# Performance work log

Hardware: AMD Instinct MI355X
Metric: run time of the kernel (lower is better)

Reference implementation:

```python
import jax, jax.numpy as jnp
import numpy as np

B, L, D, NH = 4, 1500, 512, 8
HD = D // NH
EPS = 1e-8            # F.normalize eps
PEPS = 1.1920929e-07  # torch clamp_probs eps for float32
TEMP = 1.0


def setup_inputs():
    key = jax.random.key(0)
    ks = jax.random.split(key, 12)
    s = 1.0 / np.sqrt(D)
    eye = jnp.eye(D, dtype=jnp.float32)
    return {
        "hidden": jax.random.normal(ks[0], (B, L, D), jnp.float32),
        "lengths": jnp.ones((B,), jnp.float32),
        "u_noise": jax.random.uniform(ks[1], (B, L), jnp.float32),
        "W1": jax.random.normal(ks[2], (D, D), jnp.float32) * s,
        "b1": jnp.zeros((D,), jnp.float32),
        "W2": jax.random.normal(ks[3], (D, D), jnp.float32) * s,
        "b2": jnp.zeros((D,), jnp.float32),
        "Wq": eye + jax.random.normal(ks[4], (D, D), jnp.float32) * 0.01,
        "Wk": eye + jax.random.normal(ks[5], (D, D), jnp.float32) * 0.01,
        "sim_bias": jnp.float32(0.098),
        "learned_query": jax.random.normal(ks[6], (D,), jnp.float32),
        "Wpk": eye + jax.random.normal(ks[7], (D, D), jnp.float32) * 0.01,
        "Wpv": eye + jax.random.normal(ks[8], (D, D), jnp.float32) * 0.01,
        "Wpo": eye + jax.random.normal(ks[9], (D, D), jnp.float32) * 0.01,
        "ln_g": jnp.ones((D,), jnp.float32),
        "ln_b": jnp.zeros((D,), jnp.float32),
    }


def reference(hidden, lengths, u_noise, W1, b1, W2, b2, Wq, Wk, sim_bias,
              learned_query, Wpk, Wpv, Wpo, ln_g, ln_b):
    Bb, Ll, Dd = hidden.shape

    def nrm(x):
        n = jnp.sqrt(jnp.sum(x * x, -1, keepdims=True))
        return x / jnp.maximum(n, EPS)

    def mlp(x):
        return jax.nn.gelu(x @ W1.T + b1, approximate=False) @ W2.T + b2

    # boundary logits from adjacent-frame cosine similarity (dropout = eval identity)
    q_in = nrm(hidden[:, :-1]); q = nrm(mlp(q_in) + q_in) @ Wq.T
    k_in = nrm(hidden[:, 1:]);  k = nrm(mlp(k_in) + k_in) @ Wk.T
    cos = jnp.sum(q * k, -1)                                   # (B, L-1)
    probs = jnp.clip((1.0 - (cos + sim_bias)) * 0.5, 0.0, 1.0)
    probs = jnp.pad(probs, ((0, 0), (0, 1)))                   # (B, L)

    # RelaxedBernoulli rsample with explicit logistic noise
    p = jnp.clip(probs, PEPS, 1.0 - PEPS)
    u = jnp.clip(u_noise, PEPS, 1.0 - PEPS)
    soft = jax.nn.sigmoid((jnp.log(p) - jnp.log1p(-p) + jnp.log(u) - jnp.log1p(-u)) / TEMP)
    hard = (soft > 0.5).astype(hidden.dtype)

    idx = jnp.arange(Ll)
    valid_len = jnp.minimum((lengths * (Ll + 1)).astype(jnp.int32) - 1, Ll)
    trunc = (valid_len < Ll)[:, None]
    zmask = trunc & (idx[None] >= valid_len[:, None])
    omask = trunc & (idx[None] == valid_len[:, None])
    soft = jnp.where(omask, 1.0, jnp.where(zmask, 0.0, soft))
    hard = jnp.where(omask, 1.0, jnp.where(zmask, 0.0, hard))
    hard_b = hard - jax.lax.stop_gradient(soft) + soft         # straight-through
    # emergency boundary for all-zero rows
    no_b = (jnp.sum(hard, 1) == 0)[:, None]
    hard_b = jnp.where(no_b & (idx[None] == jnp.minimum(valid_len, Ll - 1)[:, None]), 1.0, hard_b)

    # segment membership (common()): token l in segment s iff exclusive cumsum == s
    seg = jnp.cumsum(hard_b, 1) - hard_b                       # (B, L)
    lmask = idx[None] < (lengths * Ll).astype(jnp.int32)[:, None]
    seg_mask = (seg[:, :, None] == idx[None, None, :].astype(hidden.dtype)) & lmask[:, :, None]  # (B,L,S)

    # layernorm + K/V projections
    mu = jnp.mean(hidden, -1, keepdims=True)
    hv = hidden - mu
    hn = hv / jnp.sqrt(jnp.mean(hv * hv, -1, keepdims=True) + 1e-5) * ln_g + ln_b
    keys = (hn @ Wpk.T).reshape(Bb, Ll, NH, HD)
    vals = (hn @ Wpv.T).reshape(Bb, Ll, NH, HD)

    # query is shared across segments -> scores only differ via the segment mask
    qh = learned_query.reshape(NH, HD)
    base = jnp.einsum('hd,blhd->bhl', qh, keys) * (HD ** -0.5)  # (B,H,L)
    mask_t = jnp.transpose(seg_mask, (0, 2, 1))[:, None]        # (B,1,S,L)
    sc = jnp.where(mask_t, base[:, :, None, :], -jnp.inf)       # (B,H,S,L)
    aw = jnp.nan_to_num(jax.nn.softmax(sc, axis=-1))            # empty segments -> 0 rows
    pooled = jnp.einsum('bhsl,blhd->bshd', aw, vals).reshape(Bb, Ll, Dd)
    return pooled @ Wpo.T                                       # (B, S=L, D)
```

## Files before the change

kernel.cpp:

```cpp
#include <hip/hip_runtime.h>
#include <math.h>

#define Bz 4
#define Lz 1500
#define Dz 512
#define NHz 8
#define Nz (Bz*Lz)
#define PEPSf 1.1920929e-07f

typedef __bf16 bf16x8 __attribute__((ext_vector_type(8)));
typedef unsigned short u16x8 __attribute__((ext_vector_type(8)));
typedef float f32x4 __attribute__((ext_vector_type(4)));
typedef unsigned short us;

__device__ __forceinline__ us f2bf(float f) {
  unsigned u = __float_as_uint(f);
  return (us)((u + 0x7fffu + ((u >> 16) & 1u)) >> 16);
}
__device__ __forceinline__ float bf2f(us b) {
  return __uint_as_float(((unsigned)b) << 16);
}
__device__ __forceinline__ int ti_idx(int row, int col) {
  return (((row >> 4) * 64 + (col >> 3)) << 7) + ((row & 15) << 3) + (col & 7);
}
__device__ __forceinline__ void st_tiled(us* __restrict__ P, int row, int col, us v) {
  P[ti_idx(row, col)] = v;
}

__device__ __forceinline__ bool decode_blk(int bx, int ncg, int& R, int& cg) {
  int xcd = bx & 7, v = bx >> 3;
  cg = v % ncg;
  R = (v / ncg) * 8 + xcd;
  return R < 94;
}

__global__ __launch_bounds__(256) void k_wconv(
    const float* __restrict__ s0, const float* __restrict__ s1, const float* __restrict__ s2,
    const float* __restrict__ s3,
    const float* __restrict__ Wq, const float* __restrict__ Wk,
    const float* __restrict__ Wpk, const float* __restrict__ lq,
    us* __restrict__ h0, us* __restrict__ h1, us* __restrict__ h2, us* __restrict__ h3,
    us* __restrict__ l0, us* __restrict__ l1,
    us* __restrict__ WkTh, us* __restrict__ WkTl, us* __restrict__ WqTh, us* __restrict__ WqTl,
    float* __restrict__ wqe) {
  const int rt = blockIdx.x, mat = blockIdx.y, t = threadIdx.x;
  if (mat == 8) {
    if (rt < 8) {
      for (int d = t; d < Dz; d += 256) {
        float acc = 0.f;
        for (int e = 0; e < 64; ++e) acc += lq[rt * 64 + e] * Wpk[(size_t)(rt * 64 + e) * Dz + d];
        wqe[rt * Dz + d] = acc;
      }
    }
    return;
  }
  const float* S; us* H; us* L = nullptr; bool tr = false;
  switch (mat) {
    case 0: S = s0; H = h0; L = l0; break;
    case 1: S = s1; H = h1; L = l1; break;
    case 2: S = s2; H = h2; break;
    case 3: S = s3; H = h3; break;
    case 4: S = Wk; H = WkTh; L = WkTl; tr = true; break;
    default: S = Wq; H = WqTh; L = WqTl; tr = true; break;
  }
  for (int e = t; e < 8192; e += 256) {
    int mm = e >> 9, c = e & 511;
    float x = tr ? S[(size_t)c * 512 + (rt * 16 + mm)]
                 : S[(size_t)(rt * 16 + mm) * 512 + c];
    us hb = f2bf(x);
    int off = ((rt * 64 + (c >> 3)) << 7) + (mm << 3) + (c & 7);
    H[off] = hb;
    if (L) L[off] = f2bf(x - bf2f(hb));
  }
}

__global__ __launch_bounds__(256) void k_rowprep(const float* __restrict__ h,
    const float* __restrict__ g, const float* __restrict__ bb,
    const float* __restrict__ wqe,
    us* __restrict__ Uh, us* __restrict__ Ul, us* __restrict__ HNh,
    float* __restrict__ base) {
  const int row = blockIdx.x;
  const int t = threadIdx.x;
  const float* x = h + (size_t)row * Dz;
  float x0 = x[t], x1 = x[t + 256];
  float s = x0 + x1, q = x0 * x0 + x1 * x1;
  #pragma unroll
  for (int o = 32; o > 0; o >>= 1) { s += __shfl_xor(s, o, 64); q += __shfl_xor(q, o, 64); }
  __shared__ float ls[4], lq[4];
  __shared__ float xs[Dz];
  if ((t & 63) == 0) { ls[t >> 6] = s; lq[t >> 6] = q; }
  __syncthreads();
  s = ls[0] + ls[1] + ls[2] + ls[3];
  q = lq[0] + lq[1] + lq[2] + lq[3];
  float un = 1.f / fmaxf(sqrtf(q), 1e-8f);
  float u0 = x0 * un, u1 = x1 * un;
  us hb0 = f2bf(u0), hb1 = f2bf(u1);
  st_tiled(Uh, row, t, hb0);       st_tiled(Ul, row, t, f2bf(u0 - bf2f(hb0)));
  st_tiled(Uh, row, t + 256, hb1); st_tiled(Ul, row, t + 256, f2bf(u1 - bf2f(hb1)));
  float mu = s * (1.f / 512.f);
  float var = fmaxf(q * (1.f / 512.f) - mu * mu, 0.f);
  float r = rsqrtf(var + 1e-5f);
  float hn0 = (x0 - mu) * r * g[t] + bb[t];
  float hn1 = (x1 - mu) * r * g[t + 256] + bb[t + 256];
  st_tiled(HNh, row, t, f2bf(hn0));
  st_tiled(HNh, row, t + 256, f2bf(hn1));
  xs[t] = hn0; xs[t + 256] = hn1;
  __syncthreads();
  const int hh = t >> 5, lane = t & 31;
  float accb = 0.f;
  for (int d = lane; d < Dz; d += 32) accb += xs[d] * wqe[hh * Dz + d];
  #pragma unroll
  for (int o = 16; o > 0; o >>= 1) accb += __shfl_xor(accb, o, 32);
  if (lane == 0) base[(size_t)row * NHz + hh] = accb * 0.125f;
}

template<int SPLIT>
__device__ __forceinline__ void gemm_body(
    const us* __restrict__ Ah, const us* __restrict__ Al,
    const us* __restrict__ Bh, const us* __restrict__ Bl,
    const float* __restrict__ bias,
    const us* __restrict__ addH, const us* __restrict__ addL, int doGelu,
    float* __restrict__ outF, us* __restrict__ outH, us* __restrict__ outL,
    int R, int cg, int colbase, int Nrows) {
  const int t = threadIdx.x, w = t >> 6, l = t & 63;
  const int m = l & 15, q = l >> 4;
  const int wr = w & 1, wc = w >> 1;
  const int laneoff = q * 128 + m * 8;
  const int nrtm1 = (Nrows >> 4) - 1;

  const u16x8* pa[2]; const u16x8* pal[2];
  const u16x8* pb[2]; const u16x8* pbl[2];
  #pragma unroll
  for (int i = 0; i < 2; ++i) {
    int rt = min(R * 4 + wr * 2 + i, nrtm1);
    pa[i] = (const u16x8*)(Ah + (size_t)rt * 8192 + laneoff);
    if (SPLIT == 3) pal[i] = (const u16x8*)(Al + (size_t)rt * 8192 + laneoff);
  }
  #pragma unroll
  for (int j = 0; j < 2; ++j) {
    int ct = cg * 4 + wc * 2 + j;
    pb[j] = (const u16x8*)(Bh + (size_t)ct * 8192 + laneoff);
    if (SPLIT == 3) pbl[j] = (const u16x8*)(Bl + (size_t)ct * 8192 + laneoff);
  }

  u16x8 bAh[2][2], bAl[2][2], bBh[2][2], bBl[2][2];
  #pragma unroll
  for (int i = 0; i < 2; ++i) {
    bAh[0][i] = pa[i][0];
    if (SPLIT == 3) bAl[0][i] = pal[i][0];
  }
  #pragma unroll
  for (int j = 0; j < 2; ++j) {
    bBh[0][j] = pb[j][0];
    if (SPLIT == 3) bBl[0][j] = pbl[j][0];
  }

  f32x4 acc[2][2];
  #pragma unroll
  for (int i = 0; i < 2; ++i)
    #pragma unroll
    for (int j = 0; j < 2; ++j) acc[i][j] = (f32x4){0.f, 0.f, 0.f, 0.f};

  #pragma unroll 2
  for (int s = 0; s < 16; ++s) {
    const int cur = s & 1, nxt = cur ^ 1;
    const int sn = (s + 1) & 15;
    #pragma unroll
    for (int i = 0; i < 2; ++i) {
      bAh[nxt][i] = pa[i][sn * 64];
      if (SPLIT == 3) bAl[nxt][i] = pal[i][sn * 64];
    }
    #pragma unroll
    for (int j = 0; j < 2; ++j) {
      bBh[nxt][j] = pb[j][sn * 64];
      if (SPLIT == 3) bBl[nxt][j] = pbl[j][sn * 64];
    }
    #pragma unroll
    for (int i = 0; i < 2; ++i)
      #pragma unroll
      for (int j = 0; j < 2; ++j) {
        bf16x8 a = __builtin_bit_cast(bf16x8, bAh[cur][i]);
        bf16x8 b = __builtin_bit_cast(bf16x8, bBh[cur][j]);
        acc[i][j] = __builtin_amdgcn_mfma_f32_16x16x32_bf16(a, b, acc[i][j], 0, 0, 0);
        if (SPLIT == 3) {
          bf16x8 al_ = __builtin_bit_cast(bf16x8, bAl[cur][i]);
          bf16x8 bl_ = __builtin_bit_cast(bf16x8, bBl[cur][j]);
          acc[i][j] = __builtin_amdgcn_mfma_f32_16x16x32_bf16(a, bl_, acc[i][j], 0, 0, 0);
          acc[i][j] = __builtin_amdgcn_mfma_f32_16x16x32_bf16(al_, b, acc[i][j], 0, 0, 0);
        }
      }
  }

  const int row0 = R * 64 + wr * 32;
  const int col0 = colbase + wc * 32;
  #pragma unroll
  for (int i = 0; i < 2; ++i) {
    #pragma unroll
    for (int r = 0; r < 4; ++r) {
      const int grow = row0 + i * 16 + q * 4 + r;
      if (grow >= Nrows) continue;
      #pragma unroll
      for (int j = 0; j < 2; ++j) {
        const int gcol = col0 + j * 16 + m;
        float v = acc[i][j][r];
        if (bias)   v += bias[gcol];
        if (addH) {
          int ai = ti_idx(grow, gcol);
          v += bf2f(addH[ai]) + bf2f(addL[ai]);
        }
        if (doGelu) v = 0.5f * v * (1.f + erff(v * 0.70710678118654752f));
        if (outF) outF[(size_t)grow * Dz + gcol] = v;
        if (outH) {
          us hb = f2bf(v);
          st_tiled(outH, grow, gcol, hb);
          if (outL) st_tiled(outL, grow, gcol, f2bf(v - bf2f(hb)));
        }
      }
    }
  }
}

__global__ __launch_bounds__(256, 4) void g_t1_vals_gt(
    const us* Uh, const us* Ul, const us* W1h, const us* W1l, const float* b1, us* T1h, us* T1l,
    const us* HNh, const us* Wpvh, float* VALS,
    const us* WkTh, const us* WkTl, const us* WqTh, const us* WqTl, us* Gth, us* Gtl) {
  if (blockIdx.z == 2) {
    int bx = blockIdx.x;
    if (bx >= 64) return;
    gemm_body<3>(WkTh, WkTl, WqTh, WqTl, nullptr, nullptr, nullptr, 0,
                 nullptr, Gth, Gtl, bx >> 3, bx & 7, (bx & 7) * 64, 512);
    return;
  }
  int R, cg;
  if (!decode_blk(blockIdx.x, 8, R, cg)) return;
  if (blockIdx.z == 0)
    gemm_body<3>(Uh, Ul, W1h, W1l, b1, nullptr, nullptr, 1,
                 nullptr, T1h, T1l, R, cg, cg * 64, Nz);
  else
    gemm_body<1>(HNh, nullptr, Wpvh, nullptr, nullptr, nullptr, nullptr, 0,
                 VALS, nullptr, nullptr, R, cg, cg * 64, Nz);
}

__global__ __launch_bounds__(256, 4) void g_w2(
    const us* T1h, const us* T1l, const us* W2h, const us* W2l, const float* b2,
    const us* Uh, const us* Ul, float* M, us* Mh, us* Ml) {
  int R, cg;
  if (!decode_blk(blockIdx.x, 8, R, cg)) return;
  gemm_body<3>(T1h, T1l, W2h, W2l, b2, Uh, Ul, 0, M, Mh, Ml, R, cg, cg * 64, Nz);
}

__global__ __launch_bounds__(256, 4) void g_p(
    const us* Mh, const us* Ml, const us* Gth, const us* Gtl, float* P) {
  int R, cg;
  if (!decode_blk(blockIdx.x, 8, R, cg)) return;
  gemm_body<3>(Mh, Ml, Gth, Gtl, nullptr, nullptr, nullptr, 0,
               P, nullptr, nullptr, R, cg, cg * 64, Nz);
}

__global__ __launch_bounds__(256, 4) void g_out(
    const us* Ph, const us* Wpoh, float* out) {
  int R, cg;
  if (!decode_blk(blockIdx.x, 8, R, cg)) return;
  gemm_body<1>(Ph, nullptr, Wpoh, nullptr, nullptr, nullptr, nullptr, 0,
               out, nullptr, nullptr, R, cg, cg * 64, Nz);
}

__global__ __launch_bounds__(256) void k_probs(const float* __restrict__ P,
    const float* __restrict__ M, const float* __restrict__ simb,
    float* __restrict__ probs) {
  const int w = threadIdx.x >> 6, t = threadIdx.x & 63;
  const int l = blockIdx.x * 4 + w, b = blockIdx.y;
  if (l >= Lz) return;
  if (l == Lz - 1) { if (t == 0) probs[(size_t)b * Lz + l] = 0.f; return; }
  const float* pp = P + ((size_t)b * Lz + l) * Dz;
  const float* m0 = M + ((size_t)b * Lz + l) * Dz;
  const float* m1 = M + ((size_t)b * Lz + l + 1) * Dz;
  float accd = 0.f, q0 = 0.f, q1 = 0.f;
  for (int i = t; i < Dz; i += 64) {
    float a = pp[i], x0 = m0[i], x1 = m1[i];
    accd += a * x1; q0 += x0 * x0; q1 += x1 * x1;
  }
  #pragma unroll
  for (int o = 32; o > 0; o >>= 1) {
    accd += __shfl_xor(accd, o, 64);
    q0 += __shfl_xor(q0, o, 64);
    q1 += __shfl_xor(q1, o, 64);
  }
  if (t == 0) {
    float un0 = 1.f / fmaxf(sqrtf(q0), 1e-8f);
    float un1 = 1.f / fmaxf(sqrtf(q1), 1e-8f);
    float cosv = accd * un0 * un1;
    float p = (1.f - (cosv + simb[0])) * 0.5f;
    probs[(size_t)b * Lz + l] = fminf(fmaxf(p, 0.f), 1.f);
  }
}

__global__ __launch_bounds__(256) void k_boundary(const float* __restrict__ probs,
    const float* __restrict__ un, const float* __restrict__ lengths,
    int* __restrict__ seg_start, int* __restrict__ seg_meta) {
  const int b = blockIdx.x, t = threadIdx.x;
  __shared__ float hard[Lz];
  __shared__ float ps[256];
  __shared__ float ws4[4];
  const float len = lengths[b];
  const int valid_len = min((int)(len * (Lz + 1)) - 1, Lz);
  const int Lm = (int)(len * Lz);
  const bool trunc = valid_len < Lz;
  for (int l = t; l < Lz; l += 256) {
    float p = probs[(size_t)b * Lz + l];
    p = fminf(fmaxf(p, PEPSf), 1.f - PEPSf);
    float u = un[(size_t)b * Lz + l];
    u = fminf(fmaxf(u, PEPSf), 1.f - PEPSf);
    float z = logf(p) - log1pf(-p) + logf(u) - log1pf(-u);
    float soft = 1.f / (1.f + expf(-z));
    float hd = soft > 0.5f ? 1.f : 0.f;
    if (trunc && l >= valid_len) hd = (l == valid_len) ? 1.f : 0.f;
    hard[l] = hd;
  }
  __syncthreads();
  float sm = 0.f;
  for (int l = t; l < Lz; l += 256) sm += hard[l];
  #pragma unroll
  for (int o = 32; o > 0; o >>= 1) sm += __shfl_xor(sm, o, 64);
  if ((t & 63) == 0) ws4[t >> 6] = sm;
  __syncthreads();
  float total = ws4[0] + ws4[1] + ws4[2] + ws4[3];
  if (total == 0.f && t == 0) hard[min(valid_len, Lz - 1)] = 1.f;
  __syncthreads();
  const int l0 = t * 6;
  float loc = 0.f;
  for (int i = 0; i < 6; ++i) { int l = l0 + i; if (l < Lz) loc += hard[l]; }
  ps[t] = loc;
  __syncthreads();
  for (int off = 1; off < 256; off <<= 1) {
    float v = (t >= off) ? ps[t - off] : 0.f;
    __syncthreads();
    ps[t] += v;
    __syncthreads();
  }
  float run = ps[t] - loc;
  for (int i = 0; i < 6; ++i) {
    int l = l0 + i; if (l >= Lz) break;
    int seg = (int)(run + 0.5f);
    if (l == 0) seg_start[b * (Lz + 1) + 0] = 0;
    else if (hard[l - 1] > 0.5f) seg_start[b * (Lz + 1) + seg] = l;
    if (l == Lz - 1) {
      int nseg = seg + 1;
      seg_meta[b * 2 + 0] = nseg;
      seg_meta[b * 2 + 1] = Lm;
      seg_start[b * (Lz + 1) + nseg] = Lz;
    }
    run += hard[l];
  }
}

__global__ __launch_bounds__(256) void k_pool(const float* __restrict__ base,
    const float* __restrict__ VALS, const int* __restrict__ seg_start,
    const int* __restrict__ seg_meta, us* __restrict__ Ph) {
  const int s = blockIdx.x, b = blockIdx.y, t = threadIdx.x;
  const int orow = b * Lz + s;
  const int nseg = seg_meta[b * 2], Lm = seg_meta[b * 2 + 1];
  int start = 0, end = 0;
  bool empty = true;
  if (s < nseg) {
    start = seg_start[b * (Lz + 1) + s];
    end = min(seg_start[b * (Lz + 1) + s + 1], Lm);
    empty = start >= end;
  }
  if (empty) { st_tiled(Ph, orow, t, 0); st_tiled(Ph, orow, t + 256, 0); return; }
  const int h = t >> 5, lane = t & 31;
  const float* bp = base + (size_t)b * Lz * NHz + h;
  float m = -1e30f;
  for (int l = start + lane; l < end; l += 32) m = fmaxf(m, bp[(size_t)l * NHz]);
  #pragma unroll
  for (int o = 16; o > 0; o >>= 1) m = fmaxf(m, __shfl_xor(m, o, 32));
  float den = 0.f;
  for (int l = start + lane; l < end; l += 32) den += expf(bp[(size_t)l * NHz] - m);
  #pragma unroll
  for (int o = 16; o > 0; o >>= 1) den += __shfl_xor(den, o, 32);
  float a0 = 0.f, a1 = 0.f;
  const float* vp = VALS + (size_t)b * Lz * Dz + h * 64 + lane;
  for (int l = start; l < end; ++l) {
    float wgt = expf(bp[(size_t)l * NHz] - m);
    a0 += wgt * vp[(size_t)l * Dz];
    a1 += wgt * vp[(size_t)l * Dz + 32];
  }
  float inv = 1.f / den;
  st_tiled(Ph, orow, h * 64 + lane, f2bf(a0 * inv));
  st_tiled(Ph, orow, h * 64 + lane + 32, f2bf(a1 * inv));
}

extern "C" void kernel_launch(void* const* d_in, const int* in_sizes, int n_in,
                              void* d_out, int out_size, void* d_ws, size_t ws_size,
                              hipStream_t stream) {
  const float* hidden  = (const float*)d_in[0];
  const float* lengths = (const float*)d_in[1];
  const float* unoise  = (const float*)d_in[2];
  const float* W1  = (const float*)d_in[3];
  const float* b1  = (const float*)d_in[4];
  const float* W2  = (const float*)d_in[5];
  const float* b2  = (const float*)d_in[6];
  const float* Wq  = (const float*)d_in[7];
  const float* Wk  = (const float*)d_in[8];
  const float* simb   = (const float*)d_in[9];
  const float* lquery = (const float*)d_in[10];
  const float* Wpk = (const float*)d_in[11];
  const float* Wpv = (const float*)d_in[12];
  const float* Wpo = (const float*)d_in[13];
  const float* lng = (const float*)d_in[14];
  const float* lnb = (const float*)d_in[15];
  float* out = (float*)d_out;

  char* p = (char*)d_ws;
  const size_t SF = (size_t)Nz * Dz * 4;
  const size_t TP = (size_t)376 * 8192 * 2;
  const size_t WP = (size_t)32 * 8192 * 2;
  float* M    = (float*)p; p += SF;
  float* PF   = (float*)p; p += SF;
  float* VALS = (float*)p; p += SF;
  us* Uh  = (us*)p; p += TP;
  us* Ul  = (us*)p; p += TP;
  us* T1h = (us*)p; p += TP;
  us* T1l = (us*)p; p += TP;
  us* Mh  = (us*)p; p += TP;
  us* Ml  = (us*)p; p += TP;
  us* HNh = (us*)p; p += TP;
  us* Ph  = (us*)p; p += TP;
  us* W1h = (us*)p; p += WP;
  us* W1l = (us*)p; p += WP;
  us* W2h = (us*)p; p += WP;
  us* W2l = (us*)p; p += WP;
  us* Wpvh = (us*)p; p += WP;
  us* Wpoh = (us*)p; p += WP;
  us* WkTh = (us*)p; p += WP;
  us* WkTl = (us*)p; p += WP;
  us* WqTh = (us*)p; p += WP;
  us* WqTl = (us*)p; p += WP;
  us* Gth  = (us*)p; p += WP;
  us* Gtl  = (us*)p; p += WP;
  float* probs  = (float*)p; p += 24064;
  float* base   = (float*)p; p += 192000;
  int* segst    = (int*)p;   p += 24064;
  int* segmeta  = (int*)p;   p += 256;
  float* wqe    = (float*)p;

  const int G8 = 8 * 12 * 8;

  k_wconv<<<dim3(32, 9), 256, 0, stream>>>(W1, W2, Wpv, Wpo, Wq, Wk, Wpk, lquery,
      W1h, W2h, Wpvh, Wpoh, W1l, W2l, WkTh, WkTl, WqTh, WqTl, wqe);
  k_rowprep<<<Nz, 256, 0, stream>>>(hidden, lng, lnb, wqe, Uh, Ul, HNh, base);
  g_t1_vals_gt<<<dim3(G8, 1, 3), 256, 0, stream>>>(Uh, Ul, W1h, W1l, b1, T1h, T1l,
      HNh, Wpvh, VALS, WkTh, WkTl, WqTh, WqTl, Gth, Gtl);
  g_w2<<<G8, 256, 0, stream>>>(T1h, T1l, W2h, W2l, b2, Uh, Ul, M, Mh, Ml);
  g_p<<<G8, 256, 0, stream>>>(Mh, Ml, Gth, Gtl, PF);
  k_probs<<<dim3(375, Bz), 256, 0, stream>>>(PF, M, simb, probs);
  k_boundary<<<Bz, 256, 0, stream>>>(probs, unoise, lengths, segst, segmeta);
  k_pool<<<dim3(Lz, Bz), 256, 0, stream>>>(base, VALS, segst, segmeta, Ph);
  g_out<<<G8, 256, 0, stream>>>(Ph, Wpoh, out);
}
```

Before: 233.9 us.

## Merge weight conversion with row prep and compute attention scores inside pooling

The weight-conversion and row-prep kernels become one launch, with the first blocks handling weights and the rest handling rows. Because row prep no longer depends on wqe, the per-row base scores are no longer computed there. Instead k_pool recomputes each token's score from the bf16 layernormed rows (HNh) and wqe, twice per token (once for the max pass, once for the weighted sum). The denominator is also folded into the value-accumulation loop. This removes one launch and the base buffer, but it adds redundant dot products, uses bf16 instead of fp32 inputs for the scores, and uses serial per-token loops in pooling.

After: 245.4 us. +4.9%, slower.

```diff
diff --git a/kernel.cpp b/kernel.cpp
--- a/kernel.cpp
+++ b/kernel.cpp
@@ -34,64 +34,62 @@
   return R < 94;
 }
 
-__global__ __launch_bounds__(256) void k_wconv(
-    const float* __restrict__ s0, const float* __restrict__ s1, const float* __restrict__ s2,
-    const float* __restrict__ s3,
+__global__ __launch_bounds__(256) void k_prep(
+    const float* __restrict__ W1, const float* __restrict__ W2,
+    const float* __restrict__ Wpv, const float* __restrict__ Wpo,
     const float* __restrict__ Wq, const float* __restrict__ Wk,
     const float* __restrict__ Wpk, const float* __restrict__ lq,
-    us* __restrict__ h0, us* __restrict__ h1, us* __restrict__ h2, us* __restrict__ h3,
-    us* __restrict__ l0, us* __restrict__ l1,
+    const float* __restrict__ hidden, const float* __restrict__ g, const float* __restrict__ bb,
+    us* __restrict__ W1h, us* __restrict__ W2h, us* __restrict__ Wpvh, us* __restrict__ Wpoh,
+    us* __restrict__ W1l, us* __restrict__ W2l,
     us* __restrict__ WkTh, us* __restrict__ WkTl, us* __restrict__ WqTh, us* __restrict__ WqTl,
-    float* __restrict__ wqe) {
-  const int rt = blockIdx.x, mat = blockIdx.y, t = threadIdx.x;
-  if (mat == 8) {
-    if (rt < 8) {
-      for (int d = t; d < Dz; d += 256) {
-        float acc = 0.f;
-        for (int e = 0; e < 64; ++e) acc += lq[rt * 64 + e] * Wpk[(size_t)(rt * 64 + e) * Dz + d];
-        wqe[rt * Dz + d] = acc;
+    float* __restrict__ wqe,
+    us* __restrict__ Uh, us* __restrict__ Ul, us* __restrict__ HNh) {
+  const int t = threadIdx.x;
+  const int bx = blockIdx.x;
+  if (bx < 224) {
+    const int rt = bx & 31, mat = bx >> 5;
+    if (mat == 6) {
+      if (rt < 8) {
+        for (int d = t; d < Dz; d += 256) {
+          float acc = 0.f;
+          for (int e = 0; e < 64; ++e) acc += lq[rt * 64 + e] * Wpk[(size_t)(rt * 64 + e) * Dz + d];
+          wqe[rt * Dz + d] = acc;
+        }
       }
+      return;
+    }
+    const float* S; us* H; us* L = nullptr; bool tr = false;
+    switch (mat) {
+      case 0: S = W1;  H = W1h;  L = W1l; break;
+      case 1: S = W2;  H = W2h;  L = W2l; break;
+      case 2: S = Wpv; H = Wpvh; break;
+      case 3: S = Wpo; H = Wpoh; break;
+      case 4: S = Wk;  H = WkTh; L = WkTl; tr = true; break;
+      default: S = Wq; H = WqTh; L = WqTl; tr = true; break;
+    }
+    for (int e = t; e < 8192; e += 256) {
+      int mm = e >> 9, c = e & 511;
+      float x = tr ? S[(size_t)c * 512 + (rt * 16 + mm)]
+                   : S[(size_t)(rt * 16 + mm) * 512 + c];
+      us hb = f2bf(x);
+      int off = ((rt * 64 + (c >> 3)) << 7) + (mm << 3) + (c & 7);
+      H[off] = hb;
+      if (L) L[off] = f2bf(x - bf2f(hb));
     }
     return;
   }
-  const float* S; us* H; us* L = nullptr; bool tr = false;
-  switch (mat) {
-    case 0: S = s0; H = h0; L = l0; break;
-    case 1: S = s1; H = h1; L = l1; break;
-    case 2: S = s2; H = h2; break;
-    case 3: S = s3; H = h3; break;
-    case 4: S = Wk; H = WkTh; L = WkTl; tr = true; break;
-    default: S = Wq; H = WqTh; L = WqTl; tr = true; break;
-  }
-  for (int e = t; e < 8192; e += 256) {
-    int mm = e >> 9, c = e & 511;
-    float x = tr ? S[(size_t)c * 512 + (rt * 16 + mm)]
-                 : S[(size_t)(rt * 16 + mm) * 512 + c];
-    us hb = f2bf(x);
-    int off = ((rt * 64 + (c >> 3)) << 7) + (mm << 3) + (c & 7);
-    H[off] = hb;
-    if (L) L[off] = f2bf(x - bf2f(hb));
-  }
-}
-
-__global__ __launch_bounds__(256) void k_rowprep(const float* __restrict__ h,
-    const float* __restrict__ g, const float* __restrict__ bb,
-    const float* __restrict__ wqe,
-    us* __restrict__ Uh, us* __restrict__ Ul, us* __restrict__ HNh,
-    float* __restrict__ base) {
-  const int row = blockIdx.x;
-  const int t = threadIdx.x;
-  const float* x = h + (size_t)row * Dz;
+  const int row = bx - 224;
+  const float* x = hidden + (size_t)row * Dz;
   float x0 = x[t], x1 = x[t + 256];
   float s = x0 + x1, q = x0 * x0 + x1 * x1;
   #pragma unroll
   for (int o = 32; o > 0; o >>= 1) { s += __shfl_xor(s, o, 64); q += __shfl_xor(q, o, 64); }
-  __shared__ float ls[4], lq[4];
-  __shared__ float xs[Dz];
-  if ((t & 63) == 0) { ls[t >> 6] = s; lq[t >> 6] = q; }
+  __shared__ float ls[4], lqs[4];
+  if ((t & 63) == 0) { ls[t >> 6] = s; lqs[t >> 6] = q; }
   __syncthreads();
   s = ls[0] + ls[1] + ls[2] + ls[3];
-  q = lq[0] + lq[1] + lq[2] + lq[3];
+  q = lqs[0] + lqs[1] + lqs[2] + lqs[3];
   float un = 1.f / fmaxf(sqrtf(q), 1e-8f);
   float u0 = x0 * un, u1 = x1 * un;
   us hb0 = f2bf(u0), hb1 = f2bf(u1);
@@ -104,14 +102,6 @@
   float hn1 = (x1 - mu) * r * g[t + 256] + bb[t + 256];
   st_tiled(HNh, row, t, f2bf(hn0));
   st_tiled(HNh, row, t + 256, f2bf(hn1));
-  xs[t] = hn0; xs[t + 256] = hn1;
-  __syncthreads();
-  const int hh = t >> 5, lane = t & 31;
-  float accb = 0.f;
-  for (int d = lane; d < Dz; d += 32) accb += xs[d] * wqe[hh * Dz + d];
-  #pragma unroll
-  for (int o = 16; o > 0; o >>= 1) accb += __shfl_xor(accb, o, 32);
-  if (lane == 0) base[(size_t)row * NHz + hh] = accb * 0.125f;
 }
 
 template<int SPLIT>
@@ -354,7 +344,8 @@
   }
 }
 
-__global__ __launch_bounds__(256) void k_pool(const float* __restrict__ base,
+__global__ __launch_bounds__(256) void k_pool(const us* __restrict__ HNh,
+    const float* __restrict__ wqe,
     const float* __restrict__ VALS, const int* __restrict__ seg_start,
     const int* __restrict__ seg_meta, us* __restrict__ Ph) {
   const int s = blockIdx.x, b = blockIdx.y, t = threadIdx.x;
@@ -369,19 +360,30 @@
   }
   if (empty) { st_tiled(Ph, orow, t, 0); st_tiled(Ph, orow, t + 256, 0); return; }
   const int h = t >> 5, lane = t & 31;
-  const float* bp = base + (size_t)b * Lz * NHz + h;
+  float wq[16];
+  #pragma unroll
+  for (int o = 0; o < 16; ++o) wq[o] = wqe[h * Dz + o * 32 + lane];
   float m = -1e30f;
-  for (int l = start + lane; l < end; l += 32) m = fmaxf(m, bp[(size_t)l * NHz]);
-  #pragma unroll
-  for (int o = 16; o > 0; o >>= 1) m = fmaxf(m, __shfl_xor(m, o, 32));
-  float den = 0.f;
-  for (int l = start + lane; l < end; l += 32) den += expf(bp[(size_t)l * NHz] - m);
-  #pragma unroll
-  for (int o = 16; o > 0; o >>= 1) den += __shfl_xor(den, o, 32);
-  float a0 = 0.f, a1 = 0.f;
+  for (int l = start; l < end; ++l) {
+    const int grow = b * Lz + l;
+    float acc = 0.f;
+    #pragma unroll
+    for (int o = 0; o < 16; ++o) acc += bf2f(HNh[ti_idx(grow, o * 32 + lane)]) * wq[o];
+    #pragma unroll
+    for (int o2 = 16; o2 > 0; o2 >>= 1) acc += __shfl_xor(acc, o2, 32);
+    m = fmaxf(m, acc * 0.125f);
+  }
+  float den = 0.f, a0 = 0.f, a1 = 0.f;
   const float* vp = VALS + (size_t)b * Lz * Dz + h * 64 + lane;
   for (int l = start; l < end; ++l) {
-    float wgt = expf(bp[(size_t)l * NHz] - m);
+    const int grow = b * Lz + l;
+    float acc = 0.f;
+    #pragma unroll
+    for (int o = 0; o < 16; ++o) acc += bf2f(HNh[ti_idx(grow, o * 32 + lane)]) * wq[o];
+    #pragma unroll
+    for (int o2 = 16; o2 > 0; o2 >>= 1) acc += __shfl_xor(acc, o2, 32);
+    float wgt = expf(acc * 0.125f - m);
+    den += wgt;
     a0 += wgt * vp[(size_t)l * Dz];
     a1 += wgt * vp[(size_t)l * Dz + 32];
   }
@@ -439,22 +441,21 @@
   us* Gth  = (us*)p; p += WP;
   us* Gtl  = (us*)p; p += WP;
   float* probs  = (float*)p; p += 24064;
-  float* base   = (float*)p; p += 192000;
   int* segst    = (int*)p;   p += 24064;
   int* segmeta  = (int*)p;   p += 256;
   float* wqe    = (float*)p;
 
   const int G8 = 8 * 12 * 8;
 
-  k_wconv<<<dim3(32, 9), 256, 0, stream>>>(W1, W2, Wpv, Wpo, Wq, Wk, Wpk, lquery,
-      W1h, W2h, Wpvh, Wpoh, W1l, W2l, WkTh, WkTl, WqTh, WqTl, wqe);
-  k_rowprep<<<Nz, 256, 0, stream>>>(hidden, lng, lnb, wqe, Uh, Ul, HNh, base);
+  k_prep<<<224 + Nz, 256, 0, stream>>>(W1, W2, Wpv, Wpo, Wq, Wk, Wpk, lquery,
+      hidden, lng, lnb,
+      W1h, W2h, Wpvh, Wpoh, W1l, W2l, WkTh, WkTl, WqTh, WqTl, wqe, Uh, Ul, HNh);
   g_t1_vals_gt<<<dim3(G8, 1, 3), 256, 0, stream>>>(Uh, Ul, W1h, W1l, b1, T1h, T1l,
       HNh, Wpvh, VALS, WkTh, WkTl, WqTh, WqTl, Gth, Gtl);
   g_w2<<<G8, 256, 0, stream>>>(T1h, T1l, W2h, W2l, b2, Uh, Ul, M, Mh, Ml);
   g_p<<<G8, 256, 0, stream>>>(Mh, Ml, Gth, Gtl, PF);
   k_probs<<<dim3(375, Bz), 256, 0, stream>>>(PF, M, simb, probs);
   k_boundary<<<Bz, 256, 0, stream>>>(probs, unoise, lengths, segst, segmeta);
-  k_pool<<<dim3(Lz, Bz), 256, 0, stream>>>(base, VALS, segst, segmeta, Ph);
+  k_pool<<<dim3(Lz, Bz), 256, 0, stream>>>(HNh, wqe, VALS, segst, segmeta, Ph);
   g_out<<<G8, 256, 0, stream>>>(Ph, Wpoh, out);
 }
```
